# Performance work log

Hardware: AMD Instinct MI355X
Metric: run time of the kernel (lower is better)

## Reference

```python
import jax, jax.numpy as jnp
import numpy as np

N_NODES = 50000
N_EDGES = 800000
D_IN = 512
D_OUT = 256


def setup_inputs() -> dict:
    key = jax.random.key(0)
    k1, k2, k3 = jax.random.split(key, 3)
    x = jax.random.normal(k1, (N_NODES, D_IN), dtype=jnp.float32)
    edge_index = jax.random.randint(k2, (2, N_EDGES), 0, N_NODES, dtype=jnp.int64)
    # Glorot-style init for the GCN weight, zero bias (PyG defaults)
    W = jax.random.normal(k3, (D_IN, D_OUT), dtype=jnp.float32) * (1.0 / np.sqrt(D_IN))
    b = jnp.zeros((D_OUT,), dtype=jnp.float32)
    return {"x": x, "edge_index": edge_index, "W": W, "b": b}


def reference(x, edge_index, W, b):
    N = x.shape[0]
    # 1) dense linear transform (the compute-heavy GEMM)
    xw = x @ W  # [N, d_out]

    # 2) add self-loops (PyG GCNConv default)
    loop = jnp.arange(N, dtype=edge_index.dtype)
    row = jnp.concatenate([edge_index[0], loop])  # sources
    col = jnp.concatenate([edge_index[1], loop])  # targets

    # 3) symmetric normalization deg^{-1/2} on targets (in-degree incl. self-loops)
    deg = jax.ops.segment_sum(jnp.ones_like(col, dtype=xw.dtype), col, num_segments=N)
    dinv = jnp.where(deg > 0, jax.lax.rsqrt(deg), 0.0)
    norm = dinv[row] * dinv[col]  # [E+N]

    # 4) gather source features, scale, scatter-add to targets
    msgs = xw[row] * norm[:, None]  # [E+N, d_out]
    agg = jax.ops.segment_sum(msgs, col, num_segments=N)  # [N, d_out]

    # 5) bias + ReLU (dropout is identity in eval mode)
    return jax.nn.relu(agg + b)
```

## Files before the change

### kernel.cpp

```cpp
#include <hip/hip_runtime.h>
#include <hip/hip_bf16.h>

#define N_NODES 50000
#define N_EDGES 800000
#define D_IN    512
#define D_OUT   256
#define NBLK_SCAN ((N_NODES + 1023) / 1024)
#define GEMM_NWG (((N_NODES + 127) / 128) * 2)
#define GEMM_Q   (GEMM_NWG / 8)
#define GEMM_R   (GEMM_NWG % 8)

typedef short s8v  __attribute__((ext_vector_type(8)));
typedef float f32x4 __attribute__((ext_vector_type(4)));

__device__ __forceinline__ unsigned short bf16b(float f) {
    __hip_bfloat16 h = __float2bfloat16(f);
    return *reinterpret_cast<unsigned short*>(&h);
}
__device__ __forceinline__ float bflo(unsigned u) { return __uint_as_float(u << 16); }
__device__ __forceinline__ float bfhi(unsigned u) { return __uint_as_float(u & 0xffff0000u); }

#define GLD16(gp, lp)                                                           \
    __builtin_amdgcn_global_load_lds(                                           \
        (const __attribute__((address_space(1))) unsigned int*)(const void*)(gp),\
        (__attribute__((address_space(3))) unsigned int*)(void*)(lp), 16, 0, 0)

__device__ __forceinline__ int wave_incl_scan(int v, int lane) {
    #pragma unroll
    for (int d = 1; d < 64; d <<= 1) {
        int u = __shfl_up(v, d, 64);
        if (lane >= d) v += u;
    }
    return v;
}

__global__ void k_wt(const float* __restrict__ W, unsigned short* __restrict__ Wt,
                     int* __restrict__ cnt4) {
    int k = blockIdx.x;
    int n = threadIdx.x;
    Wt[(size_t)n * D_IN + k] = bf16b(W[(size_t)k * D_OUT + n]);
    int t = (blockIdx.x * 256 + threadIdx.x) * 2;
    if (t < 4 * N_NODES) {
        cnt4[t] = 0;
        if (t + 1 < 4 * N_NODES) cnt4[t + 1] = 0;
    }
}


__global__ void k_count(const int* __restrict__ col, int* __restrict__ cnt4) {
    int i = (blockIdx.x * 256 + threadIdx.x) * 2;
    if (i < N_EDGES) {
        int2 c = *(const int2*)&col[i];
        atomicAdd(&cnt4[(i & 3) * N_NODES + c.x], 1);
        atomicAdd(&cnt4[((i + 1) & 3) * N_NODES + c.y], 1);
    }
}

__launch_bounds__(256)
__global__ void k_scan1(const int* __restrict__ cnt4, int* __restrict__ bsum) {
    const int t = threadIdx.x, b = blockIdx.x;
    const int idx = b * 1024 + t * 4;
    int s = 0;
    if (idx < N_NODES) {
        #pragma unroll
        for (int q = 0; q < 4; ++q) {
            int4 v = *(const int4*)&cnt4[q * N_NODES + idx];
            s += (v.x + v.y) + (v.z + v.w);
        }
    }
    #pragma unroll
    for (int d = 1; d < 64; d <<= 1) s += __shfl_xor(s, d, 64);
    __shared__ int ws[4];
    if ((t & 63) == 0) ws[t >> 6] = s;
    __syncthreads();
    if (t == 0) bsum[b] = ws[0] + ws[1] + ws[2] + ws[3];
}

__launch_bounds__(256)
__global__ void k_scan3(const int* __restrict__ cnt4, const int* __restrict__ bsum,
                        int* __restrict__ row_ptr, float* __restrict__ dinv,
                        int* __restrict__ cursor4) {
    const int t = threadIdx.x, b = blockIdx.x;
    const int lane = t & 63, wv = t >> 6;
    const int idx = b * 1024 + t * 4;
    int4 vq[4];
    int4 tot = make_int4(0, 0, 0, 0);
    if (idx < N_NODES) {
        #pragma unroll
        for (int q = 0; q < 4; ++q) {
            vq[q] = *(const int4*)&cnt4[q * N_NODES + idx];
            tot.x += vq[q].x; tot.y += vq[q].y;
            tot.z += vq[q].z; tot.w += vq[q].w;
        }
    } else {
        #pragma unroll
        for (int q = 0; q < 4; ++q) vq[q] = make_int4(0, 0, 0, 0);
    }
    int s = (tot.x + tot.y) + (tot.z + tot.w);
    int isc = wave_incl_scan(s, lane);
    __shared__ int wsum[4];
    __shared__ int s_boff;
    if (lane == 63) wsum[wv] = isc;
    if (t < 64) {
        int u = (t < b) ? bsum[t] : 0;
        #pragma unroll
        for (int d = 1; d < 64; d <<= 1) u += __shfl_xor(u, d, 64);
        if (t == 0) s_boff = u;
    }
    __syncthreads();
    int off = s_boff;
    #pragma unroll
    for (int i = 0; i < 4; ++i)
        if (i < wv) off += wsum[i];
    int p0 = off + isc - s;
    int p1 = p0 + tot.x;
    int p2 = p1 + tot.y;
    int p3 = p2 + tot.z;
    if (idx < N_NODES) {
        row_ptr[idx + 0] = p0; dinv[idx + 0] = rsqrtf(1.f + (float)tot.x);
        row_ptr[idx + 1] = p1; dinv[idx + 1] = rsqrtf(1.f + (float)tot.y);
        row_ptr[idx + 2] = p2; dinv[idx + 2] = rsqrtf(1.f + (float)tot.z);
        row_ptr[idx + 3] = p3; dinv[idx + 3] = rsqrtf(1.f + (float)tot.w);
        int4 run = make_int4(p0, p1, p2, p3);
        #pragma unroll
        for (int q = 0; q < 4; ++q) {
            *(int4*)&cursor4[q * N_NODES + idx] = run;
            run.x += vq[q].x; run.y += vq[q].y;
            run.z += vq[q].z; run.w += vq[q].w;
        }
    }
    if (b == 0 && t == 0) row_ptr[N_NODES] = N_EDGES;
}

__global__ void k_fill(const int* __restrict__ row, const int* __restrict__ col,
                       int* __restrict__ cursor4, int* __restrict__ csr_src) {
    int i = (blockIdx.x * 256 + threadIdx.x) * 2;
    if (i < N_EDGES) {
        int2 c = *(const int2*)&col[i];
        int2 r = *(const int2*)&row[i];
        int p0 = atomicAdd(&cursor4[(i & 3) * N_NODES + c.x], 1);
        csr_src[p0] = r.x;
        int p1 = atomicAdd(&cursor4[((i + 1) & 3) * N_NODES + c.y], 1);
        csr_src[p1] = r.y;
    }
}

__launch_bounds__(256)
__global__ void k_gemm(const float* __restrict__ A,
                       const unsigned short* __restrict__ Wt,
                       const float* __restrict__ dinv,
                       unsigned short* __restrict__ yb)
{
    __shared__ __align__(16) float          As[128 * 64];
    __shared__ __align__(16) unsigned short Bs[128 * 64];

    int orig = blockIdx.x;
    int xcd = orig % 8, pos = orig / 8;
    int wg = (xcd < GEMM_R) ? xcd * (GEMM_Q + 1) + pos
                            : GEMM_R * (GEMM_Q + 1) + (xcd - GEMM_R) * GEMM_Q + pos;
    const int nt = wg & 1;
    const int mt = wg >> 1;
    const int m0 = mt * 128;
    const int n0 = nt * 128;

    const int t  = threadIdx.x;
    const int w  = t >> 6;
    const int l  = t & 63;
    const int wm = (w >> 1) * 64;
    const int wn = (w & 1) * 64;
    const int lr = l & 15;
    const int lk = l >> 4;

    size_t aoff[8];
    #pragma unroll
    for (int i = 0; i < 8; ++i) {
        int row = m0 + w * 32 + i * 4 + (l >> 4);
        if (row >= N_NODES) row = 0;
        int sslot = (l & 15) ^ (row & 7);
        aoff[i] = (size_t)row * D_IN + sslot * 4;
    }
    const int srow = l >> 3;
    const int srcj = (l & 7) ^ srow;
    size_t boff[4];
    #pragma unroll
    for (int i = 0; i < 4; ++i) {
        int g = w * 4 + i;
        int bn = n0 + g * 8 + srow;
        boff[i] = (size_t)bn * D_IN + srcj * 8;
    }

    f32x4 acc[4][4] = {};

    for (int kk = 0; kk < D_IN; kk += 64) {
        #pragma unroll
        for (int i = 0; i < 8; ++i)
            GLD16(&A[aoff[i] + kk], (char*)As + (w * 32 + i * 4) * 256);
        #pragma unroll
        for (int i = 0; i < 4; ++i)
            GLD16(&Wt[boff[i] + kk], (char*)Bs + (w * 4 + i) * 1024);
        __syncthreads();

        #pragma unroll
        for (int ks = 0; ks < 2; ++ks) {
            s8v af[4], bfr[4];
            #pragma unroll
            for (int f = 0; f < 4; ++f) {
                int row = wm + f * 16 + lr;
                int a   = (ks * 4 + lk) * 2;
                int s0  = a ^ (lr & 7);
                int s1  = (a + 1) ^ (lr & 7);
                const char* pr = (const char*)As + row * 256;
                float4 x0 = *(const float4*)(pr + s0 * 16);
                float4 x1 = *(const float4*)(pr + s1 * 16);
                union { s8v v; unsigned short h[8]; } u;
                u.h[0] = bf16b(x0.x); u.h[1] = bf16b(x0.y);
                u.h[2] = bf16b(x0.z); u.h[3] = bf16b(x0.w);
                u.h[4] = bf16b(x1.x); u.h[5] = bf16b(x1.y);
                u.h[6] = bf16b(x1.z); u.h[7] = bf16b(x1.w);
                af[f] = u.v;
            }
            const int kb = (ks * 64 + lk * 16) ^ ((lr & 7) << 4);
            #pragma unroll
            for (int f = 0; f < 4; ++f)
                bfr[f] = *(const s8v*)((const char*)Bs + ((wn + f * 16 + lr) * 128 + kb));
            #pragma unroll
            for (int fm = 0; fm < 4; ++fm)
                #pragma unroll
                for (int fn = 0; fn < 4; ++fn)
                    acc[fm][fn] = __builtin_amdgcn_mfma_f32_16x16x32_bf16(
                        af[fm], bfr[fn], acc[fm][fn], 0, 0, 0);
        }
        __syncthreads();
    }

    #pragma unroll
    for (int fm = 0; fm < 4; ++fm) {
        #pragma unroll
        for (int j = 0; j < 4; ++j) {
            int row = m0 + wm + fm * 16 + lk * 4 + j;
            if (row < N_NODES) {
                float s = dinv[row];
                #pragma unroll
                for (int fn = 0; fn < 4; ++fn) {
                    int col = n0 + wn + fn * 16 + lr;
                    yb[(size_t)row * D_OUT + col] = bf16b(acc[fm][fn][j] * s);
                }
            }
        }
    }
}

__device__ __forceinline__ void add8(float* acc, uint4 q) {
    unsigned x;
    x = q.x; acc[0] += bflo(x); acc[1] += bfhi(x);
    x = q.y; acc[2] += bflo(x); acc[3] += bfhi(x);
    x = q.z; acc[4] += bflo(x); acc[5] += bfhi(x);
    x = q.w; acc[6] += bflo(x); acc[7] += bfhi(x);
}

__launch_bounds__(256)
__global__ void k_gather(const int* __restrict__ row_ptr, const int* __restrict__ csr_src,
                         const unsigned short* __restrict__ yb, const float* __restrict__ dinv,
                         const float* __restrict__ bias, float* __restrict__ out)
{
    const int c  = blockIdx.x * 4 + (threadIdx.x >> 6);
    const int l  = threadIdx.x & 63;
    const int eg = l >> 5;
    const int cs = l & 31;
    const size_t colb = (size_t)cs * 8;

    float acc[8] = {0.f,0.f,0.f,0.f,0.f,0.f,0.f,0.f};

    const int s = row_ptr[c];
    const int e = row_ptr[c + 1];

    int i = s + eg;
    while (i + 14 < e) {
        int r[8];
        #pragma unroll
        for (int u = 0; u < 8; ++u) r[u] = csr_src[i + 2 * u];
        uint4 v[8];
        #pragma unroll
        for (int u = 0; u < 8; ++u) v[u] = *(const uint4*)&yb[(size_t)r[u] * D_OUT + colb];
        #pragma unroll
        for (int u = 0; u < 8; ++u) add8(acc, v[u]);
        i += 16;
    }
    while (i < e) {
        int r[4];
        #pragma unroll
        for (int u = 0; u < 4; ++u) {
            int p = i + 2 * u;
            r[u] = csr_src[p < e ? p : e - 1];
        }
        uint4 v[4];
        #pragma unroll
        for (int u = 0; u < 4; ++u) v[u] = *(const uint4*)&yb[(size_t)r[u] * D_OUT + colb];
        #pragma unroll
        for (int u = 0; u < 4; ++u)
            if (i + 2 * u < e) add8(acc, v[u]);
        i += 8;
    }

    #pragma unroll
    for (int u = 0; u < 8; ++u) acc[u] += __shfl_xor(acc[u], 32, 64);

    uint4 sv = *(const uint4*)&yb[(size_t)c * D_OUT + colb];
    add8(acc, sv);

    if (eg == 0) {
        const float sc = dinv[c];
        float4 b0 = *(const float4*)&bias[colb];
        float4 b1 = *(const float4*)&bias[colb + 4];
        float4 o0, o1;
        o0.x = fmaxf(fmaf(acc[0], sc, b0.x), 0.f);
        o0.y = fmaxf(fmaf(acc[1], sc, b0.y), 0.f);
        o0.z = fmaxf(fmaf(acc[2], sc, b0.z), 0.f);
        o0.w = fmaxf(fmaf(acc[3], sc, b0.w), 0.f);
        o1.x = fmaxf(fmaf(acc[4], sc, b1.x), 0.f);
        o1.y = fmaxf(fmaf(acc[5], sc, b1.y), 0.f);
        o1.z = fmaxf(fmaf(acc[6], sc, b1.z), 0.f);
        o1.w = fmaxf(fmaf(acc[7], sc, b1.w), 0.f);
        float* dst = &out[(size_t)c * D_OUT + colb];
        *(float4*)dst       = o0;
        *(float4*)(dst + 4) = o1;
    }
}

extern "C" void kernel_launch(void* const* d_in, const int* in_sizes, int n_in,
                              void* d_out, int out_size, void* d_ws, size_t ws_size,
                              hipStream_t stream) {
    const float* x   = (const float*)d_in[0];
    const int*   ei  = (const int*)d_in[1];
    const float* W   = (const float*)d_in[2];
    const float* b   = (const float*)d_in[3];
    float*       out = (float*)d_out;

    const int* row = ei;
    const int* col = ei + N_EDGES;

    char* p = (char*)d_ws;
    unsigned short* yb = (unsigned short*)p;  p += (size_t)N_NODES * D_OUT * 2;
    unsigned short* Wt = (unsigned short*)p;  p += (size_t)D_OUT * D_IN * 2;
    int*   csr_src = (int*)p;                 p += (size_t)N_EDGES * 4;
    int*   cnt4    = (int*)p;                 p += (size_t)4 * N_NODES * 4;
    int*   row_ptr = (int*)p;                 p += (size_t)(N_NODES + 4) * 4;
    int*   cursor4 = (int*)p;                 p += (size_t)4 * N_NODES * 4;
    float* dinv    = (float*)p;               p += (size_t)N_NODES * 4;
    int*   bsum    = (int*)p;                 p += (size_t)NBLK_SCAN * 4;

    k_wt   <<<D_IN, D_OUT, 0, stream>>>(W, Wt, cnt4);
    k_count<<<(N_EDGES / 2 + 255) / 256, 256, 0, stream>>>(col, cnt4);
    k_scan1<<<NBLK_SCAN, 256, 0, stream>>>(cnt4, bsum);
    k_scan3<<<NBLK_SCAN, 256, 0, stream>>>(cnt4, bsum, row_ptr, dinv, cursor4);
    k_fill <<<(N_EDGES / 2 + 255) / 256, 256, 0, stream>>>(row, col, cursor4, csr_src);

    k_gemm<<<GEMM_NWG, 256, 0, stream>>>(x, Wt, dinv, yb);

    k_gather<<<N_NODES / 4, 256, 0, stream>>>(row_ptr, csr_src, yb, dinv, b, out);
}
```

Baseline: 193.5 us.

## Slice GEMM output into column panels and gather per panel for cache locality

Result: no change. 192.6 us (-0.5%).

```diff
diff --git a/kernel.cpp b/kernel.cpp
--- a/kernel.cpp
+++ b/kernel.cpp
@@ -9,6 +9,7 @@
 #define GEMM_NWG (((N_NODES + 127) / 128) * 2)
 #define GEMM_Q   (GEMM_NWG / 8)
 #define GEMM_R   (GEMM_NWG % 8)
+#define GATH_CHUNKS ((N_NODES + 63) / 64)
 
 typedef short s8v  __attribute__((ext_vector_type(8)));
 typedef float f32x4 __attribute__((ext_vector_type(4)));
@@ -243,7 +244,9 @@
                 #pragma unroll
                 for (int fn = 0; fn < 4; ++fn) {
                     int col = n0 + wn + fn * 16 + lr;
-                    yb[(size_t)row * D_OUT + col] = bf16b(acc[fm][fn][j] * s);
+                    size_t off = (size_t)(col >> 5) * (N_NODES * 32)
+                               + (size_t)row * 32 + (col & 31);
+                    yb[off] = bf16b(acc[fm][fn][j] * s);
                 }
             }
         }
@@ -260,71 +263,56 @@
 
 __launch_bounds__(256)
 __global__ void k_gather(const int* __restrict__ row_ptr, const int* __restrict__ csr_src,
-                         const unsigned short* __restrict__ yb, const float* __restrict__ dinv,
+                         const unsigned short* __restrict__ yb,
+                         const float* __restrict__ dinv,
                          const float* __restrict__ bias, float* __restrict__ out)
 {
-    const int c  = blockIdx.x * 4 + (threadIdx.x >> 6);
-    const int l  = threadIdx.x & 63;
-    const int eg = l >> 5;
-    const int cs = l & 31;
-    const size_t colb = (size_t)cs * 8;
+    const int s     = blockIdx.x & 7;
+    const int chunk = blockIdx.x >> 3;
+    const int g     = threadIdx.x >> 2;
+    const int cs    = threadIdx.x & 3;
+    const int c     = chunk * 64 + g;
+    if (c >= N_NODES) return;
+
+    const uint4* t4 = (const uint4*)(yb + (size_t)s * N_NODES * 32);
 
     float acc[8] = {0.f,0.f,0.f,0.f,0.f,0.f,0.f,0.f};
 
-    const int s = row_ptr[c];
-    const int e = row_ptr[c + 1];
-
-    int i = s + eg;
-    while (i + 14 < e) {
-        int r[8];
-        #pragma unroll
-        for (int u = 0; u < 8; ++u) r[u] = csr_src[i + 2 * u];
-        uint4 v[8];
-        #pragma unroll
-        for (int u = 0; u < 8; ++u) v[u] = *(const uint4*)&yb[(size_t)r[u] * D_OUT + colb];
-        #pragma unroll
-        for (int u = 0; u < 8; ++u) add8(acc, v[u]);
-        i += 16;
-    }
-    while (i < e) {
-        int r[4];
-        #pragma unroll
-        for (int u = 0; u < 4; ++u) {
-            int p = i + 2 * u;
-            r[u] = csr_src[p < e ? p : e - 1];
+    const int e0 = row_ptr[c];
+    const int e1 = row_ptr[c + 1];
+    for (int i = e0; i < e1; i += 4) {
+        int idx[4];
+        #pragma unroll
+        for (int j = 0; j < 4; ++j) {
+            int p = i + j;
+            idx[j] = csr_src[p < e1 ? p : e1 - 1];
         }
         uint4 v[4];
         #pragma unroll
-        for (int u = 0; u < 4; ++u) v[u] = *(const uint4*)&yb[(size_t)r[u] * D_OUT + colb];
-        #pragma unroll
-        for (int u = 0; u < 4; ++u)
-            if (i + 2 * u < e) add8(acc, v[u]);
-        i += 8;
-    }
-
-    #pragma unroll
-    for (int u = 0; u < 8; ++u) acc[u] += __shfl_xor(acc[u], 32, 64);
-
-    uint4 sv = *(const uint4*)&yb[(size_t)c * D_OUT + colb];
-    add8(acc, sv);
-
-    if (eg == 0) {
-        const float sc = dinv[c];
-        float4 b0 = *(const float4*)&bias[colb];
-        float4 b1 = *(const float4*)&bias[colb + 4];
-        float4 o0, o1;
-        o0.x = fmaxf(fmaf(acc[0], sc, b0.x), 0.f);
-        o0.y = fmaxf(fmaf(acc[1], sc, b0.y), 0.f);
-        o0.z = fmaxf(fmaf(acc[2], sc, b0.z), 0.f);
-        o0.w = fmaxf(fmaf(acc[3], sc, b0.w), 0.f);
-        o1.x = fmaxf(fmaf(acc[4], sc, b1.x), 0.f);
-        o1.y = fmaxf(fmaf(acc[5], sc, b1.y), 0.f);
-        o1.z = fmaxf(fmaf(acc[6], sc, b1.z), 0.f);
-        o1.w = fmaxf(fmaf(acc[7], sc, b1.w), 0.f);
-        float* dst = &out[(size_t)c * D_OUT + colb];
-        *(float4*)dst       = o0;
-        *(float4*)(dst + 4) = o1;
-    }
+        for (int j = 0; j < 4; ++j) v[j] = t4[(size_t)idx[j] * 4 + cs];
+        #pragma unroll
+        for (int j = 0; j < 4; ++j)
+            if (i + j < e1) add8(acc, v[j]);
+    }
+
+    add8(acc, t4[(size_t)c * 4 + cs]);
+
+    const float sc = dinv[c];
+    const int colb = s * 32 + cs * 8;
+    float4 b0 = *(const float4*)&bias[colb];
+    float4 b1 = *(const float4*)&bias[colb + 4];
+    float4 o0, o1;
+    o0.x = fmaxf(fmaf(acc[0], sc, b0.x), 0.f);
+    o0.y = fmaxf(fmaf(acc[1], sc, b0.y), 0.f);
+    o0.z = fmaxf(fmaf(acc[2], sc, b0.z), 0.f);
+    o0.w = fmaxf(fmaf(acc[3], sc, b0.w), 0.f);
+    o1.x = fmaxf(fmaf(acc[4], sc, b1.x), 0.f);
+    o1.y = fmaxf(fmaf(acc[5], sc, b1.y), 0.f);
+    o1.z = fmaxf(fmaf(acc[6], sc, b1.z), 0.f);
+    o1.w = fmaxf(fmaf(acc[7], sc, b1.w), 0.f);
+    float* dst = &out[(size_t)c * D_OUT + colb];
+    *(float4*)dst       = o0;
+    *(float4*)(dst + 4) = o1;
 }
 
 extern "C" void kernel_launch(void* const* d_in, const int* in_sizes, int n_in,
@@ -357,5 +345,5 @@
 
     k_gemm<<<GEMM_NWG, 256, 0, stream>>>(x, Wt, dinv, yb);
 
-    k_gather<<<N_NODES / 4, 256, 0, stream>>>(row_ptr, csr_src, yb, dinv, b, out);
-}
+    k_gather<<<GATH_CHUNKS * 8, 256, 0, stream>>>(row_ptr, csr_src, yb, dinv, b, out);
+}
```
